# Kernel tuning notes

Hardware: AMD Instinct MI355X
Metric: run time of the kernel (lower is better)

Reference implementation:

```python
import jax, jax.numpy as jnp
import numpy as np

N = 100000  # nodes
E = 1600000  # edges
F_IN = 512
H = 128
C = 40
L = 8
ALPHA = 0.1
THETA = 0.5


def setup_inputs() -> dict:
    key = jax.random.key(0)
    ks = jax.random.split(key, 8)
    x = jax.random.normal(ks[0], (N, F_IN), dtype=jnp.float32)
    edge_index = jax.random.randint(ks[1], (2, E), 0, N, dtype=jnp.int32)
    edge_weight = jax.random.uniform(ks[2], (E,), dtype=jnp.float32)
    W0 = jax.random.normal(ks[3], (F_IN, H), dtype=jnp.float32) * 0.05
    b0 = jnp.zeros((H,), dtype=jnp.float32)
    convW = jax.random.normal(ks[4], (L, H, H), dtype=jnp.float32) * 0.05
    W1 = jax.random.normal(ks[5], (H, C), dtype=jnp.float32) * 0.05
    b1 = jnp.zeros((C,), dtype=jnp.float32)
    return {"x": x, "edge_index": edge_index, "edge_weight": edge_weight,
            "W0": W0, "b0": b0, "convW": convW, "W1": W1, "b1": b1}


def reference(x, edge_index, edge_weight, W0, b0, convW, W1, b1):
    # eval mode, dropout=0.0 -> dropout is identity
    src, dst = edge_index[0], edge_index[1]
    h = jnp.maximum(x @ W0 + b0, 0.0)  # [N, H]
    x0 = h  # initial residual
    # GCN2Conv beta per layer: log(theta/layer + 1), layer = 1..L
    betas = jnp.log(THETA / jnp.arange(1, L + 1, dtype=jnp.float32) + 1.0)

    def layer(h, inputs):
        W, beta = inputs  # W: [H, H]
        # sparse adjacency propagation: sum_j A_ij * h_j
        msgs = h[src] * edge_weight[:, None]  # [E, H]
        agg = jax.ops.segment_sum(msgs, dst, num_segments=N)  # [N, H]
        # initial residual mixing + identity mapping (shared_weights=True)
        out = (1.0 - ALPHA) * agg + ALPHA * x0
        out = (1.0 - beta) * out + beta * (out @ W)
        return jnp.maximum(out, 0.0), None

    h, _ = jax.lax.scan(layer, h, (convW, betas))
    logits = h @ W1 + b1  # [N, C]
    return jax.nn.log_softmax(logits, axis=-1)
```

## Files before the change

kernel.cpp:

```cpp
#include <hip/hip_runtime.h>
#include <hip/hip_bf16.h>
#include <cmath>

#define NN 100000
#define NE 1600000
#define FIN 512
#define HD 128
#define NC 40
#define NL 8
#define NBK 196
#define P1B 256
#define CHUNK ((NE + P1B - 1) / P1B)

typedef __attribute__((ext_vector_type(8))) short bh8;
typedef __attribute__((ext_vector_type(4))) float f4;
typedef __attribute__((ext_vector_type(4))) unsigned int u4;
typedef __attribute__((ext_vector_type(2))) unsigned int u2;

__device__ __forceinline__ float bflo(unsigned p){ return __uint_as_float(p << 16); }
__device__ __forceinline__ float bfhi(unsigned p){ return __uint_as_float(p & 0xffff0000u); }
__device__ __forceinline__ unsigned short f2bf(float f){
  unsigned u = __float_as_uint(f);
  u += 0x7fffu + ((u >> 16) & 1u);
  return (unsigned short)(u >> 16);
}
__device__ __forceinline__ unsigned pack2(float a, float b){
  return (unsigned)f2bf(a) | ((unsigned)f2bf(b) << 16);
}

__global__ __launch_bounds__(256) void k_hist(const int* __restrict__ dst,
                                              int* __restrict__ bcnt){
  __shared__ int h[256];
  int t = threadIdx.x;
  h[t] = 0;
  __syncthreads();
  int lo = blockIdx.x * CHUNK;
  int hi = lo + CHUNK < NE ? lo + CHUNK : NE;
  for (int i = lo + t; i < hi; i += 256)
    atomicAdd(&h[dst[i] >> 9], 1);
  __syncthreads();
  if (h[t]) atomicAdd(&bcnt[t], h[t]);
}

__global__ void k_bscan(const int* __restrict__ bcnt, int* __restrict__ gbase,
                        int* __restrict__ gcur, int* __restrict__ offs){
  int t = threadIdx.x;
  int carry = 0;
  for (int base = 0; base < 256; base += 64){
    int v = bcnt[base + t];
    int orig = v;
    #pragma unroll
    for (int off = 1; off < 64; off <<= 1){
      int u = __shfl_up(v, off);
      if (t >= off) v += u;
    }
    int excl = carry + v - orig;
    gbase[base + t] = excl;
    gcur[base + t] = excl;
    carry += __shfl(v, 63);
  }
  if (t == 0){ gbase[256] = carry; offs[NN] = NE; }
}

__global__ __launch_bounds__(256) void k_part(const int* __restrict__ src,
                                              const int* __restrict__ dst,
                                              const float* __restrict__ w,
                                              int* __restrict__ gcur,
                                              u2* __restrict__ tmp){
  __shared__ int h[256];
  __shared__ int base[256];
  int t = threadIdx.x;
  h[t] = 0;
  __syncthreads();
  int lo = blockIdx.x * CHUNK;
  int hi = lo + CHUNK < NE ? lo + CHUNK : NE;
  for (int i = lo + t; i < hi; i += 256)
    atomicAdd(&h[dst[i] >> 9], 1);
  __syncthreads();
  int cnt = h[t];
  if (cnt) base[t] = atomicAdd(&gcur[t], cnt);
  h[t] = 0;
  __syncthreads();
  for (int i = lo + t; i < hi; i += 256){
    int d = dst[i];
    int bk = d >> 9;
    int r = atomicAdd(&h[bk], 1);
    u2 v = { (unsigned)src[i] | ((unsigned)(d & 511) << 17), __float_as_uint(w[i]) };
    tmp[base[bk] + r] = v;
  }
}

__global__ __launch_bounds__(256) void k_place(const u2* __restrict__ tmp,
                                               const int* __restrict__ gbase,
                                               int* __restrict__ offs,
                                               u2* __restrict__ epk){
  __shared__ int h[512];
  __shared__ int lofs[512];
  int b = blockIdx.x;
  int t = threadIdx.x;
  int e0 = gbase[b], e1 = gbase[b + 1];
  h[t] = 0; h[t + 256] = 0;
  __syncthreads();
  for (int i = e0 + t; i < e1; i += 256)
    atomicAdd(&h[tmp[i].x >> 17], 1);
  __syncthreads();
  if (t < 64){
    int carry = 0;
    for (int base = 0; base < 512; base += 64){
      int v = h[base + t];
      int orig = v;
      #pragma unroll
      for (int off = 1; off < 64; off <<= 1){
        int u = __shfl_up(v, off);
        if (t >= off) v += u;
      }
      lofs[base + t] = carry + v - orig;
      carry += __shfl(v, 63);
    }
  }
  __syncthreads();
  int d = b * 512 + t;
  if (d < NN) offs[d] = e0 + lofs[t];
  int d2 = b * 512 + 256 + t;
  if (d2 < NN) offs[d2] = e0 + lofs[256 + t];
  h[t] = 0; h[t + 256] = 0;
  __syncthreads();
  for (int i = e0 + t; i < e1; i += 256){
    u2 v = tmp[i];
    int d9 = v.x >> 17;
    int r = atomicAdd(&h[d9], 1);
    u2 o = { v.x & 0x1FFFFu, v.y };
    epk[e0 + lofs[d9] + r] = o;
  }
}

__global__ void k_twt_all(const float* __restrict__ W0, const float* __restrict__ cW,
                          const float* __restrict__ W1, unsigned short* __restrict__ out){
  const int n0 = FIN * HD;
  const int n1 = NL * HD * HD;
  const int total = n0 + n1 + 48 * HD;
  for (int i = blockIdx.x * blockDim.x + threadIdx.x; i < total; i += gridDim.x * blockDim.x){
    float v;
    if (i < n0){
      int c = i / FIN, k = i % FIN;
      v = W0[(size_t)k * HD + c];
    } else if (i < n0 + n1){
      int j = i - n0;
      int l = j / (HD * HD), r = j % (HD * HD);
      int c = r / HD, k = r % HD;
      v = cW[(size_t)l * HD * HD + k * HD + c];
    } else {
      int j = i - n0 - n1;
      int c = j / HD, k = j % HD;
      v = (c < NC) ? W1[(size_t)k * NC + c] : 0.f;
    }
    out[i] = f2bf(v);
  }
}

__global__ __launch_bounds__(256) void k_gemm0(const float* __restrict__ X,
                                               const unsigned short* __restrict__ Wt,
                                               const float* __restrict__ b0,
                                               unsigned* __restrict__ Ha,
                                               unsigned* __restrict__ Hb, int n){
  __shared__ __attribute__((aligned(16))) char lds[33792];
  char* ldsA = lds;
  char* ldsW = lds + 8192;
  float* ldsO = (float*)lds;
  int t = threadIdx.x;
  int w = t >> 6, lane = t & 63;
  int rowBase = blockIdx.x * 64;
  f4 acc[8];
  #pragma unroll
  for (int i = 0; i < 8; i++) acc[i] = (f4)0.f;

  for (int kk = 0; kk < 8; kk++){
    #pragma unroll
    for (int iter = 0; iter < 2; iter++){
      int r = t / 8 + iter * 32;
      int kc = (t % 8) * 8;
      int grow = rowBase + r;
      float4 f0 = {0,0,0,0}, f1 = {0,0,0,0};
      if (grow < n){
        const float4* p = (const float4*)(X + (size_t)grow * FIN + kk * 64 + kc);
        f0 = p[0]; f1 = p[1];
      }
      u4 pv = { pack2(f0.x, f0.y), pack2(f0.z, f0.w), pack2(f1.x, f1.y), pack2(f1.z, f1.w) };
      *(u4*)(ldsA + r * 128 + ((kc * 2) ^ ((r & 7) << 4))) = pv;
    }
    #pragma unroll
    for (int iter = 0; iter < 4; iter++){
      int c = t / 8 + iter * 32;
      int kc = (t % 8) * 8;
      bh8 v = *(const bh8*)(Wt + (size_t)c * FIN + kk * 64 + kc);
      *(bh8*)(ldsW + c * 128 + ((kc * 2) ^ ((c & 7) << 4))) = v;
    }
    __syncthreads();
    int rowf = (w << 4) + (lane & 15);
    #pragma unroll
    for (int ks = 0; ks < 2; ks++){
      bh8 fa = *(const bh8*)(ldsA + rowf * 128 + ((ks * 64 + (lane >> 4) * 16) ^ ((rowf & 7) << 4)));
      #pragma unroll
      for (int ct = 0; ct < 8; ct++){
        int colf = (ct << 4) + (lane & 15);
        bh8 fb = *(const bh8*)(ldsW + colf * 128 + ((ks * 64 + (lane >> 4) * 16) ^ ((colf & 7) << 4)));
        acc[ct] = __builtin_amdgcn_mfma_f32_16x16x32_bf16(fa, fb, acc[ct], 0, 0, 0);
      }
    }
    __syncthreads();
  }
  #pragma unroll
  for (int ct = 0; ct < 8; ct++){
    int colf = (ct << 4) + (lane & 15);
    float bb = b0[colf];
    #pragma unroll
    for (int i = 0; i < 4; i++){
      int r = (w << 4) + ((lane >> 4) << 2) + i;
      float v = acc[ct][i] + bb;
      ldsO[r * 132 + colf] = v > 0.f ? v : 0.f;
    }
  }
  __syncthreads();
  #pragma unroll
  for (int iter = 0; iter < 4; iter++){
    int r = iter * 16 + t / 16;
    int c8 = (t % 16) * 8;
    int grow = rowBase + r;
    if (grow < n){
      float* p = &ldsO[r * 132 + c8];
      u4 pv = { pack2(p[0], p[1]), pack2(p[2], p[3]), pack2(p[4], p[5]), pack2(p[6], p[7]) };
      *(u4*)(Ha + (size_t)grow * 64 + (t % 16) * 4) = pv;
      *(u4*)(Hb + (size_t)grow * 64 + (t % 16) * 4) = pv;
    }
  }
}

__global__ __launch_bounds__(512) void k_layer(const unsigned* __restrict__ Hin,
                                               const unsigned* __restrict__ X0,
                                               const int* __restrict__ offs,
                                               const u2* __restrict__ epk,
                                               const unsigned short* __restrict__ Wt,
                                               float beta,
                                               unsigned* __restrict__ Hout, int n){
  __shared__ __attribute__((aligned(16))) char ldsA[16384];
  int t = threadIdx.x;
  int w = t >> 6, lane = t & 63;
  int q = lane >> 4, l16 = lane & 15;
  int quadId = (w << 2) + q;
  int rowBase = blockIdx.x * 64;

  #pragma unroll
  for (int rr = 0; rr < 2; rr++){
    int lr = (quadId << 1) + rr;
    int d = rowBase + lr;
    bool act = d < n;
    int e0 = act ? offs[d] : 0;
    int e1 = act ? offs[d + 1] : 0;
    float a0=0.f,a1=0.f,a2=0.f,a3=0.f,a4=0.f,a5=0.f,a6=0.f,a7=0.f;
    int e = e0;
    for (; e + 7 < e1; e += 8){
      #pragma unroll
      for (int j = 0; j < 8; j++){
        u2 pe = epk[e + j];
        float wf = __uint_as_float(pe.y);
        u4 r = *(const u4*)(Hin + (size_t)pe.x * 64 + l16 * 4);
        a0 += wf * bflo(r.x); a1 += wf * bfhi(r.x);
        a2 += wf * bflo(r.y); a3 += wf * bfhi(r.y);
        a4 += wf * bflo(r.z); a5 += wf * bfhi(r.z);
        a6 += wf * bflo(r.w); a7 += wf * bfhi(r.w);
      }
    }
    for (; e < e1; e++){
      u2 pe = epk[e];
      float wf = __uint_as_float(pe.y);
      u4 r = *(const u4*)(Hin + (size_t)pe.x * 64 + l16 * 4);
      a0 += wf * bflo(r.x); a1 += wf * bfhi(r.x);
      a2 += wf * bflo(r.y); a3 += wf * bfhi(r.y);
      a4 += wf * bflo(r.z); a5 += wf * bfhi(r.z);
      a6 += wf * bflo(r.w); a7 += wf * bfhi(r.w);
    }
    u4 ov = { 0u, 0u, 0u, 0u };
    if (act){
      u4 xp = *(const u4*)(X0 + (size_t)d * 64 + l16 * 4);
      float v0 = 0.9f*a0 + 0.1f*bflo(xp.x), v1 = 0.9f*a1 + 0.1f*bfhi(xp.x);
      float v2 = 0.9f*a2 + 0.1f*bflo(xp.y), v3 = 0.9f*a3 + 0.1f*bfhi(xp.y);
      float v4 = 0.9f*a4 + 0.1f*bflo(xp.z), v5 = 0.9f*a5 + 0.1f*bfhi(xp.z);
      float v6 = 0.9f*a6 + 0.1f*bflo(xp.w), v7 = 0.9f*a7 + 0.1f*bfhi(xp.w);
      ov = (u4){ pack2(v0,v1), pack2(v2,v3), pack2(v4,v5), pack2(v6,v7) };
    }
    *(u4*)(ldsA + lr * 256 + ((l16 * 16) ^ ((lr & 7) << 4))) = ov;
  }
  __syncthreads();

  f4 acc[4];
  #pragma unroll
  for (int i = 0; i < 4; i++) acc[i] = (f4)0.f;
  int rowf = ((w & 3) << 4) + l16;
  int colBase = (w >> 2) << 6;
  #pragma unroll
  for (int ks = 0; ks < 4; ks++){
    bh8 fa = *(const bh8*)(ldsA + rowf * 256 + ((ks * 64 + q * 16) ^ ((rowf & 7) << 4)));
    #pragma unroll
    for (int ct = 0; ct < 4; ct++){
      int colf = colBase + (ct << 4) + l16;
      bh8 fb = *(const bh8*)(Wt + (size_t)colf * HD + ks * 32 + q * 8);
      acc[ct] = __builtin_amdgcn_mfma_f32_16x16x32_bf16(fa, fb, acc[ct], 0, 0, 0);
    }
  }

  #pragma unroll
  for (int ct = 0; ct < 4; ct++){
    int colf = colBase + (ct << 4) + l16;
    #pragma unroll
    for (int i = 0; i < 4; i++){
      int r = ((w & 3) << 4) + (q << 2) + i;
      char* addr = ldsA + r * 256 + ((colf * 2) ^ ((r & 7) << 4));
      unsigned short tv = *(const unsigned short*)addr;
      float tf = __uint_as_float(((unsigned)tv) << 16);
      float v = (1.f - beta) * tf + beta * acc[ct][i];
      *(unsigned short*)addr = f2bf(v > 0.f ? v : 0.f);
    }
  }
  __syncthreads();

  #pragma unroll
  for (int iter = 0; iter < 2; iter++){
    int r = iter * 32 + t / 16;
    int kc = (t % 16) * 8;
    int grow = rowBase + r;
    if (grow < n){
      bh8 v = *(const bh8*)(ldsA + r * 256 + ((kc * 2) ^ ((r & 7) << 4)));
      *(bh8*)((unsigned short*)Hout + (size_t)grow * HD + kc) = v;
    }
  }
}

__global__ __launch_bounds__(256) void k_final(const unsigned* __restrict__ H,
                                               const unsigned short* __restrict__ W1t,
                                               const float* __restrict__ b1,
                                               float* __restrict__ out, int n){
  __shared__ __attribute__((aligned(16))) char lds[16384 + 12288];
  char* ldsA = lds;
  char* ldsW = lds + 16384;
  int t = threadIdx.x;
  int w = t >> 6, lane = t & 63;
  int l15 = lane & 15;
  int rowBase = blockIdx.x * 64;
  const unsigned short* Hs = (const unsigned short*)H;

  #pragma unroll
  for (int iter = 0; iter < 4; iter++){
    int r = t / 16 + iter * 16;
    int kc = (t % 16) * 8;
    int grow = rowBase + r;
    bh8 v = (bh8)(short)0;
    if (grow < n) v = *(const bh8*)(Hs + (size_t)grow * HD + kc);
    *(bh8*)(ldsA + r * 256 + ((kc * 2) ^ ((r & 7) << 4))) = v;
  }
  #pragma unroll
  for (int iter = 0; iter < 3; iter++){
    int c = t / 16 + iter * 16;
    int kc = (t % 16) * 8;
    bh8 v = *(const bh8*)(W1t + (size_t)c * HD + kc);
    *(bh8*)(ldsW + c * 256 + ((kc * 2) ^ ((c & 7) << 4))) = v;
  }
  __syncthreads();

  f4 acc[3];
  #pragma unroll
  for (int i = 0; i < 3; i++) acc[i] = (f4)0.f;
  int rowf = (w << 4) + l15;
  #pragma unroll
  for (int ks = 0; ks < 4; ks++){
    bh8 fa = *(const bh8*)(ldsA + rowf * 256 + ((ks * 64 + (lane >> 4) * 16) ^ ((rowf & 7) << 4)));
    #pragma unroll
    for (int ct = 0; ct < 3; ct++){
      int colf = (ct << 4) + l15;
      bh8 fb = *(const bh8*)(ldsW + colf * 256 + ((ks * 64 + (lane >> 4) * 16) ^ ((colf & 7) << 4)));
      acc[ct] = __builtin_amdgcn_mfma_f32_16x16x32_bf16(fa, fb, acc[ct], 0, 0, 0);
    }
  }

  float bias0 = b1[l15];
  float bias1 = b1[16 + l15];
  bool v2ok = (l15 < 8);
  float bias2 = v2ok ? b1[32 + l15] : 0.f;

  #pragma unroll
  for (int i = 0; i < 4; i++){
    int r = rowBase + (w << 4) + ((lane >> 4) << 2) + i;
    float v0 = acc[0][i] + bias0;
    float v1 = acc[1][i] + bias1;
    float v2 = v2ok ? (acc[2][i] + bias2) : -1e30f;
    float m = fmaxf(fmaxf(v0, v1), v2);
    #pragma unroll
    for (int off = 1; off < 16; off <<= 1) m = fmaxf(m, __shfl_xor(m, off));
    float e0 = __expf(v0 - m), e1 = __expf(v1 - m);
    float e2 = v2ok ? __expf(v2 - m) : 0.f;
    float s = e0 + e1 + e2;
    #pragma unroll
    for (int off = 1; off < 16; off <<= 1) s += __shfl_xor(s, off);
    float ls = m + __logf(s);
    if (r < n){
      out[(size_t)r * NC + l15] = v0 - ls;
      out[(size_t)r * NC + 16 + l15] = v1 - ls;
      if (v2ok) out[(size_t)r * NC + 32 + l15] = v2 - ls;
    }
  }
}

extern "C" void kernel_launch(void* const* d_in, const int* in_sizes, int n_in,
                              void* d_out, int out_size, void* d_ws, size_t ws_size,
                              hipStream_t stream){
  const float* x  = (const float*)d_in[0];
  const int*   ei = (const int*)d_in[1];
  const float* ew = (const float*)d_in[2];
  const float* W0 = (const float*)d_in[3];
  const float* b0 = (const float*)d_in[4];
  const float* cW = (const float*)d_in[5];
  const float* W1 = (const float*)d_in[6];
  const float* b1 = (const float*)d_in[7];
  float* out = (float*)d_out;
  const int* src = ei;
  const int* dst = ei + NE;

  char* ws = (char*)d_ws;
  size_t off = 0;
  auto alloc = [&](size_t bytes) -> char* {
    char* p = ws + off;
    off += (bytes + 255) & ~(size_t)255;
    return p;
  };
  unsigned* x0b = (unsigned*)alloc((size_t)NN * 64 * 4);
  unsigned* hbA = (unsigned*)alloc((size_t)NN * 64 * 4);
  unsigned* hbB = (unsigned*)alloc((size_t)NN * 64 * 4);
  unsigned short* wbuf = (unsigned short*)alloc(((size_t)FIN * HD + (size_t)NL * HD * HD + 48 * HD) * 2);
  unsigned short* W0t = wbuf;
  unsigned short* cWt = wbuf + (size_t)FIN * HD;
  unsigned short* W1t = cWt + (size_t)NL * HD * HD;
  int*   offs  = (int*)alloc((size_t)(NN + 1) * 4);
  int*   bcnt  = (int*)alloc(256 * 4);
  int*   gbase = (int*)alloc(257 * 4);
  int*   gcur  = (int*)alloc(256 * 4);
  u2*    tmp   = (u2*)alloc((size_t)NE * 8);
  u2*    epk   = (u2*)alloc((size_t)NE * 8);

  (void)hipMemsetAsync(bcnt, 0, 256 * 4, stream);
  hipLaunchKernelGGL(k_hist, dim3(P1B), dim3(256), 0, stream, dst, bcnt);
  hipLaunchKernelGGL(k_bscan, dim3(1), dim3(64), 0, stream, bcnt, gbase, gcur, offs);
  hipLaunchKernelGGL(k_part, dim3(P1B), dim3(256), 0, stream, src, dst, ew, gcur, tmp);
  hipLaunchKernelGGL(k_place, dim3(NBK), dim3(256), 0, stream, tmp, gbase, offs, epk);
  hipLaunchKernelGGL(k_twt_all, dim3(256), dim3(256), 0, stream, W0, cW, W1, wbuf);

  int gblocks = (NN + 63) / 64;
  hipLaunchKernelGGL(k_gemm0, dim3(gblocks), dim3(256), 0, stream, x, W0t, b0, x0b, hbA, NN);
  for (int l = 0; l < NL; l++){
    float beta = logf(0.5f / (float)(l + 1) + 1.0f);
    const unsigned* hin = (l & 1) ? hbB : hbA;
    unsigned* hout = (l & 1) ? hbA : hbB;
    hipLaunchKernelGGL(k_layer, dim3(gblocks), dim3(512), 0, stream,
                       hin, x0b, offs, epk, cWt + (size_t)l * HD * HD, beta, hout, NN);
  }
  hipLaunchKernelGGL(k_final, dim3(gblocks), dim3(256), 0, stream, hbA, W1t, b1, out, NN);
}
```

Baseline: 1.000 ms.

## Slice hidden features into 8 column planes and split aggregation from layer GEMM

Hidden and residual buffers are stored as 8 column slices of 16 features each (32 bytes per node), so each aggregation block gathers one slice. The slice-major order of blocks is meant to keep one slice's 3.2 MB working set resident in cache during the random gather. The fused per-layer kernel becomes a gather-only kernel that writes an intermediate buffer and a separate MFMA GEMM kernel that reads it back. This adds a kernel launch and an extra write and read of the intermediate per layer. Gathers also become 4-byte loads per lane instead of 16-byte vectors.

```diff
diff --git a/kernel.cpp b/kernel.cpp
--- a/kernel.cpp
+++ b/kernel.cpp
@@ -11,6 +11,8 @@
 #define NBK 196
 #define P1B 256
 #define CHUNK ((NE + P1B - 1) / P1B)
+#define ATILE 512
+#define NTILE ((NN + ATILE - 1) / ATILE)
 
 typedef __attribute__((ext_vector_type(8))) short bh8;
 typedef __attribute__((ext_vector_type(4))) float f4;
@@ -221,99 +223,105 @@
     }
   }
   __syncthreads();
-  #pragma unroll
-  for (int iter = 0; iter < 4; iter++){
-    int r = iter * 16 + t / 16;
-    int c8 = (t % 16) * 8;
-    int grow = rowBase + r;
+  int r2 = t >> 2, p = t & 3;
+  #pragma unroll
+  for (int s = 0; s < 8; s++){
+    int grow = rowBase + r2;
     if (grow < n){
-      float* p = &ldsO[r * 132 + c8];
-      u4 pv = { pack2(p[0], p[1]), pack2(p[2], p[3]), pack2(p[4], p[5]), pack2(p[6], p[7]) };
-      *(u4*)(Ha + (size_t)grow * 64 + (t % 16) * 4) = pv;
-      *(u4*)(Hb + (size_t)grow * 64 + (t % 16) * 4) = pv;
-    }
-  }
-}
-
-__global__ __launch_bounds__(512) void k_layer(const unsigned* __restrict__ Hin,
-                                               const unsigned* __restrict__ X0,
-                                               const int* __restrict__ offs,
-                                               const u2* __restrict__ epk,
+      float* pp = &ldsO[r2 * 132 + s * 16 + p * 4];
+      u2 pv = { pack2(pp[0], pp[1]), pack2(pp[2], pp[3]) };
+      *(u2*)(Ha + (size_t)s * NN * 8 + (size_t)grow * 8 + p * 2) = pv;
+      *(u2*)(Hb + (size_t)s * NN * 8 + (size_t)grow * 8 + p * 2) = pv;
+    }
+  }
+}
+
+__global__ __launch_bounds__(256) void k_agg(const unsigned* __restrict__ Hs,
+                                             const unsigned* __restrict__ X0s,
+                                             const int* __restrict__ offs,
+                                             const u2* __restrict__ epk,
+                                             unsigned* __restrict__ Ts, int n){
+  int b = blockIdx.x;
+  int s = b & 7;
+  int tile = b >> 3;
+  int t = threadIdx.x;
+  int g = t >> 3;
+  int j = t & 7;
+  const unsigned* Hb = Hs + (size_t)s * NN * 8;
+  const unsigned* Xb = X0s + (size_t)s * NN * 8;
+  unsigned* Tb = Ts + (size_t)s * NN * 8;
+  int d0 = tile * ATILE + g * 16;
+  #pragma unroll 1
+  for (int dd = 0; dd < 16; dd++){
+    int d = d0 + dd;
+    if (d >= n) break;
+    int e0 = offs[d], e1 = offs[d + 1];
+    float ax = 0.f, ay = 0.f;
+    int e = e0;
+    for (; e + 3 < e1; e += 4){
+      u2 p0 = epk[e], p1 = epk[e + 1], p2 = epk[e + 2], p3 = epk[e + 3];
+      unsigned h0 = Hb[(size_t)p0.x * 8 + j];
+      unsigned h1 = Hb[(size_t)p1.x * 8 + j];
+      unsigned h2 = Hb[(size_t)p2.x * 8 + j];
+      unsigned h3 = Hb[(size_t)p3.x * 8 + j];
+      float w0 = __uint_as_float(p0.y), w1 = __uint_as_float(p1.y);
+      float w2 = __uint_as_float(p2.y), w3 = __uint_as_float(p3.y);
+      ax += w0*bflo(h0) + w1*bflo(h1) + w2*bflo(h2) + w3*bflo(h3);
+      ay += w0*bfhi(h0) + w1*bfhi(h1) + w2*bfhi(h2) + w3*bfhi(h3);
+    }
+    for (; e < e1; e++){
+      u2 pe = epk[e];
+      unsigned h = Hb[(size_t)pe.x * 8 + j];
+      float wf = __uint_as_float(pe.y);
+      ax += wf * bflo(h); ay += wf * bfhi(h);
+    }
+    unsigned xv = Xb[(size_t)d * 8 + j];
+    float vx = 0.9f * ax + 0.1f * bflo(xv);
+    float vy = 0.9f * ay + 0.1f * bfhi(xv);
+    Tb[(size_t)d * 8 + j] = pack2(vx, vy);
+  }
+}
+
+__global__ __launch_bounds__(256) void k_gemmL(const unsigned* __restrict__ Ts,
                                                const unsigned short* __restrict__ Wt,
                                                float beta,
-                                               unsigned* __restrict__ Hout, int n){
+                                               unsigned* __restrict__ Hs, int n){
   __shared__ __attribute__((aligned(16))) char ldsA[16384];
   int t = threadIdx.x;
   int w = t >> 6, lane = t & 63;
   int q = lane >> 4, l16 = lane & 15;
-  int quadId = (w << 2) + q;
   int rowBase = blockIdx.x * 64;
-
-  #pragma unroll
-  for (int rr = 0; rr < 2; rr++){
-    int lr = (quadId << 1) + rr;
-    int d = rowBase + lr;
-    bool act = d < n;
-    int e0 = act ? offs[d] : 0;
-    int e1 = act ? offs[d + 1] : 0;
-    float a0=0.f,a1=0.f,a2=0.f,a3=0.f,a4=0.f,a5=0.f,a6=0.f,a7=0.f;
-    int e = e0;
-    for (; e + 7 < e1; e += 8){
-      #pragma unroll
-      for (int j = 0; j < 8; j++){
-        u2 pe = epk[e + j];
-        float wf = __uint_as_float(pe.y);
-        u4 r = *(const u4*)(Hin + (size_t)pe.x * 64 + l16 * 4);
-        a0 += wf * bflo(r.x); a1 += wf * bfhi(r.x);
-        a2 += wf * bflo(r.y); a3 += wf * bfhi(r.y);
-        a4 += wf * bflo(r.z); a5 += wf * bfhi(r.z);
-        a6 += wf * bflo(r.w); a7 += wf * bfhi(r.w);
-      }
-    }
-    for (; e < e1; e++){
-      u2 pe = epk[e];
-      float wf = __uint_as_float(pe.y);
-      u4 r = *(const u4*)(Hin + (size_t)pe.x * 64 + l16 * 4);
-      a0 += wf * bflo(r.x); a1 += wf * bfhi(r.x);
-      a2 += wf * bflo(r.y); a3 += wf * bfhi(r.y);
-      a4 += wf * bflo(r.z); a5 += wf * bfhi(r.z);
-      a6 += wf * bflo(r.w); a7 += wf * bfhi(r.w);
-    }
-    u4 ov = { 0u, 0u, 0u, 0u };
-    if (act){
-      u4 xp = *(const u4*)(X0 + (size_t)d * 64 + l16 * 4);
-      float v0 = 0.9f*a0 + 0.1f*bflo(xp.x), v1 = 0.9f*a1 + 0.1f*bfhi(xp.x);
-      float v2 = 0.9f*a2 + 0.1f*bflo(xp.y), v3 = 0.9f*a3 + 0.1f*bfhi(xp.y);
-      float v4 = 0.9f*a4 + 0.1f*bflo(xp.z), v5 = 0.9f*a5 + 0.1f*bfhi(xp.z);
-      float v6 = 0.9f*a6 + 0.1f*bflo(xp.w), v7 = 0.9f*a7 + 0.1f*bfhi(xp.w);
-      ov = (u4){ pack2(v0,v1), pack2(v2,v3), pack2(v4,v5), pack2(v6,v7) };
-    }
-    *(u4*)(ldsA + lr * 256 + ((l16 * 16) ^ ((lr & 7) << 4))) = ov;
-  }
-  __syncthreads();
-
-  f4 acc[4];
-  #pragma unroll
-  for (int i = 0; i < 4; i++) acc[i] = (f4)0.f;
-  int rowf = ((w & 3) << 4) + l16;
-  int colBase = (w >> 2) << 6;
+  int r2 = t >> 2, p = t & 3;
+
+  #pragma unroll
+  for (int s = 0; s < 8; s++){
+    int grow = rowBase + r2;
+    u2 v = { 0u, 0u };
+    if (grow < n) v = *(const u2*)(Ts + (size_t)s * NN * 8 + (size_t)grow * 8 + p * 2);
+    *(u2*)(ldsA + r2 * 256 + ((s * 32 + p * 8) ^ ((r2 & 7) << 4))) = v;
+  }
+
+  f4 acc[8];
+  #pragma unroll
+  for (int i = 0; i < 8; i++) acc[i] = (f4)0.f;
+  int rowf = (w << 4) + l16;
   #pragma unroll
   for (int ks = 0; ks < 4; ks++){
     bh8 fa = *(const bh8*)(ldsA + rowf * 256 + ((ks * 64 + q * 16) ^ ((rowf & 7) << 4)));
     #pragma unroll
-    for (int ct = 0; ct < 4; ct++){
-      int colf = colBase + (ct << 4) + l16;
+    for (int ct = 0; ct < 8; ct++){
+      int colf = (ct << 4) + l16;
       bh8 fb = *(const bh8*)(Wt + (size_t)colf * HD + ks * 32 + q * 8);
       acc[ct] = __builtin_amdgcn_mfma_f32_16x16x32_bf16(fa, fb, acc[ct], 0, 0, 0);
     }
   }
 
   #pragma unroll
-  for (int ct = 0; ct < 4; ct++){
-    int colf = colBase + (ct << 4) + l16;
+  for (int ct = 0; ct < 8; ct++){
+    int colf = (ct << 4) + l16;
     #pragma unroll
     for (int i = 0; i < 4; i++){
-      int r = ((w & 3) << 4) + (q << 2) + i;
+      int r = (w << 4) + (q << 2) + i;
       char* addr = ldsA + r * 256 + ((colf * 2) ^ ((r & 7) << 4));
       unsigned short tv = *(const unsigned short*)addr;
       float tf = __uint_as_float(((unsigned)tv) << 16);
@@ -324,18 +332,16 @@
   __syncthreads();
 
   #pragma unroll
-  for (int iter = 0; iter < 2; iter++){
-    int r = iter * 32 + t / 16;
-    int kc = (t % 16) * 8;
-    int grow = rowBase + r;
+  for (int s = 0; s < 8; s++){
+    int grow = rowBase + r2;
     if (grow < n){
-      bh8 v = *(const bh8*)(ldsA + r * 256 + ((kc * 2) ^ ((r & 7) << 4)));
-      *(bh8*)((unsigned short*)Hout + (size_t)grow * HD + kc) = v;
-    }
-  }
-}
-
-__global__ __launch_bounds__(256) void k_final(const unsigned* __restrict__ H,
+      u2 v = *(const u2*)(ldsA + r2 * 256 + ((s * 32 + p * 8) ^ ((r2 & 7) << 4)));
+      *(u2*)(Hs + (size_t)s * NN * 8 + (size_t)grow * 8 + p * 2) = v;
+    }
+  }
+}
+
+__global__ __launch_bounds__(256) void k_final(const unsigned* __restrict__ Hs,
                                                const unsigned short* __restrict__ W1t,
                                                const float* __restrict__ b1,
                                                float* __restrict__ out, int n){
@@ -346,16 +352,14 @@
   int w = t >> 6, lane = t & 63;
   int l15 = lane & 15;
   int rowBase = blockIdx.x * 64;
-  const unsigned short* Hs = (const unsigned short*)H;
-
-  #pragma unroll
-  for (int iter = 0; iter < 4; iter++){
-    int r = t / 16 + iter * 16;
-    int kc = (t % 16) * 8;
-    int grow = rowBase + r;
-    bh8 v = (bh8)(short)0;
-    if (grow < n) v = *(const bh8*)(Hs + (size_t)grow * HD + kc);
-    *(bh8*)(ldsA + r * 256 + ((kc * 2) ^ ((r & 7) << 4))) = v;
+  int r2 = t >> 2, p = t & 3;
+
+  #pragma unroll
+  for (int s = 0; s < 8; s++){
+    int grow = rowBase + r2;
+    u2 v = { 0u, 0u };
+    if (grow < n) v = *(const u2*)(Hs + (size_t)s * NN * 8 + (size_t)grow * 8 + p * 2);
+    *(u2*)(ldsA + r2 * 256 + ((s * 32 + p * 8) ^ ((r2 & 7) << 4))) = v;
   }
   #pragma unroll
   for (int iter = 0; iter < 3; iter++){
@@ -434,6 +438,7 @@
   unsigned* x0b = (unsigned*)alloc((size_t)NN * 64 * 4);
   unsigned* hbA = (unsigned*)alloc((size_t)NN * 64 * 4);
   unsigned* hbB = (unsigned*)alloc((size_t)NN * 64 * 4);
+  unsigned* tb  = (unsigned*)alloc((size_t)NN * 64 * 4);
   unsigned short* wbuf = (unsigned short*)alloc(((size_t)FIN * HD + (size_t)NL * HD * HD + 48 * HD) * 2);
   unsigned short* W0t = wbuf;
   unsigned short* cWt = wbuf + (size_t)FIN * HD;
@@ -458,8 +463,10 @@
     float beta = logf(0.5f / (float)(l + 1) + 1.0f);
     const unsigned* hin = (l & 1) ? hbB : hbA;
     unsigned* hout = (l & 1) ? hbA : hbB;
-    hipLaunchKernelGGL(k_layer, dim3(gblocks), dim3(512), 0, stream,
-                       hin, x0b, offs, epk, cWt + (size_t)l * HD * HD, beta, hout, NN);
+    hipLaunchKernelGGL(k_agg, dim3(NTILE * 8), dim3(256), 0, stream,
+                       hin, x0b, offs, epk, tb, NN);
+    hipLaunchKernelGGL(k_gemmL, dim3(gblocks), dim3(256), 0, stream,
+                       tb, cWt + (size_t)l * HD * HD, beta, hout, NN);
   }
   hipLaunchKernelGGL(k_final, dim3(gblocks), dim3(256), 0, stream, hbA, W1t, b1, out, NN);
 }
```

Result: slower. 1.550 ms (+55.0%).

## Split fused layer kernel into grid-stride aggregation and separate MFMA GEMM

Applied to the files above, without the earlier changes.

The fused per-layer kernel (gather-aggregate into LDS, then MFMA transform) is split into two kernels. k_agg is a persistent grid-stride kernel with one 16-lane group per node, using no LDS and no barriers. It writes the residual-mixed bf16 result to a new global buffer. k_gemmL reads that buffer into LDS and runs the 128x128 transform with each wave covering all output columns. This aims to free the memory-bound gather from the GEMM's LDS, barrier and occupancy limits and to balance irregular degrees better. The cost is an extra global write and read of an N×128 bf16 tensor plus a second launch per layer.

```diff
diff --git a/kernel.cpp b/kernel.cpp
--- a/kernel.cpp
+++ b/kernel.cpp
@@ -235,27 +235,17 @@
   }
 }
 
-__global__ __launch_bounds__(512) void k_layer(const unsigned* __restrict__ Hin,
-                                               const unsigned* __restrict__ X0,
-                                               const int* __restrict__ offs,
-                                               const u2* __restrict__ epk,
-                                               const unsigned short* __restrict__ Wt,
-                                               float beta,
-                                               unsigned* __restrict__ Hout, int n){
-  __shared__ __attribute__((aligned(16))) char ldsA[16384];
-  int t = threadIdx.x;
-  int w = t >> 6, lane = t & 63;
-  int q = lane >> 4, l16 = lane & 15;
-  int quadId = (w << 2) + q;
-  int rowBase = blockIdx.x * 64;
-
-  #pragma unroll
-  for (int rr = 0; rr < 2; rr++){
-    int lr = (quadId << 1) + rr;
-    int d = rowBase + lr;
-    bool act = d < n;
-    int e0 = act ? offs[d] : 0;
-    int e1 = act ? offs[d + 1] : 0;
+__global__ __launch_bounds__(256) void k_agg(const unsigned* __restrict__ H,
+                                             const unsigned* __restrict__ X0,
+                                             const int* __restrict__ offs,
+                                             const u2* __restrict__ epk,
+                                             unsigned* __restrict__ T, int n){
+  int t = threadIdx.x;
+  int qid = (blockIdx.x << 4) + (t >> 4);
+  int l16 = t & 15;
+  int nq = gridDim.x << 4;
+  for (int d = qid; d < n; d += nq){
+    int e0 = offs[d], e1 = offs[d + 1];
     float a0=0.f,a1=0.f,a2=0.f,a3=0.f,a4=0.f,a5=0.f,a6=0.f,a7=0.f;
     int e = e0;
     for (; e + 7 < e1; e += 8){
@@ -263,7 +253,7 @@
       for (int j = 0; j < 8; j++){
         u2 pe = epk[e + j];
         float wf = __uint_as_float(pe.y);
-        u4 r = *(const u4*)(Hin + (size_t)pe.x * 64 + l16 * 4);
+        u4 r = *(const u4*)(H + (size_t)pe.x * 64 + l16 * 4);
         a0 += wf * bflo(r.x); a1 += wf * bfhi(r.x);
         a2 += wf * bflo(r.y); a3 += wf * bfhi(r.y);
         a4 += wf * bflo(r.z); a5 += wf * bfhi(r.z);
@@ -273,47 +263,63 @@
     for (; e < e1; e++){
       u2 pe = epk[e];
       float wf = __uint_as_float(pe.y);
-      u4 r = *(const u4*)(Hin + (size_t)pe.x * 64 + l16 * 4);
+      u4 r = *(const u4*)(H + (size_t)pe.x * 64 + l16 * 4);
       a0 += wf * bflo(r.x); a1 += wf * bfhi(r.x);
       a2 += wf * bflo(r.y); a3 += wf * bfhi(r.y);
       a4 += wf * bflo(r.z); a5 += wf * bfhi(r.z);
       a6 += wf * bflo(r.w); a7 += wf * bfhi(r.w);
     }
-    u4 ov = { 0u, 0u, 0u, 0u };
-    if (act){
-      u4 xp = *(const u4*)(X0 + (size_t)d * 64 + l16 * 4);
-      float v0 = 0.9f*a0 + 0.1f*bflo(xp.x), v1 = 0.9f*a1 + 0.1f*bfhi(xp.x);
-      float v2 = 0.9f*a2 + 0.1f*bflo(xp.y), v3 = 0.9f*a3 + 0.1f*bfhi(xp.y);
-      float v4 = 0.9f*a4 + 0.1f*bflo(xp.z), v5 = 0.9f*a5 + 0.1f*bfhi(xp.z);
-      float v6 = 0.9f*a6 + 0.1f*bflo(xp.w), v7 = 0.9f*a7 + 0.1f*bfhi(xp.w);
-      ov = (u4){ pack2(v0,v1), pack2(v2,v3), pack2(v4,v5), pack2(v6,v7) };
-    }
-    *(u4*)(ldsA + lr * 256 + ((l16 * 16) ^ ((lr & 7) << 4))) = ov;
-  }
-  __syncthreads();
-
-  f4 acc[4];
-  #pragma unroll
-  for (int i = 0; i < 4; i++) acc[i] = (f4)0.f;
-  int rowf = ((w & 3) << 4) + l16;
-  int colBase = (w >> 2) << 6;
+    u4 xp = *(const u4*)(X0 + (size_t)d * 64 + l16 * 4);
+    float v0 = 0.9f*a0 + 0.1f*bflo(xp.x), v1 = 0.9f*a1 + 0.1f*bfhi(xp.x);
+    float v2 = 0.9f*a2 + 0.1f*bflo(xp.y), v3 = 0.9f*a3 + 0.1f*bfhi(xp.y);
+    float v4 = 0.9f*a4 + 0.1f*bflo(xp.z), v5 = 0.9f*a5 + 0.1f*bfhi(xp.z);
+    float v6 = 0.9f*a6 + 0.1f*bflo(xp.w), v7 = 0.9f*a7 + 0.1f*bfhi(xp.w);
+    u4 ov = { pack2(v0,v1), pack2(v2,v3), pack2(v4,v5), pack2(v6,v7) };
+    *(u4*)(T + (size_t)d * 64 + l16 * 4) = ov;
+  }
+}
+
+__global__ __launch_bounds__(256) void k_gemmL(const unsigned short* __restrict__ A,
+                                               const unsigned short* __restrict__ Wt,
+                                               float beta,
+                                               unsigned* __restrict__ Hout, int n){
+  __shared__ __attribute__((aligned(16))) char ldsA[16384];
+  int t = threadIdx.x;
+  int w = t >> 6, lane = t & 63;
+  int q = lane >> 4, l16 = lane & 15;
+  int rowBase = blockIdx.x * 64;
+
+  #pragma unroll
+  for (int it = 0; it < 4; it++){
+    int lr = (w << 4) + (lane >> 2);
+    int j = it * 4 + (lane & 3);
+    int grow = rowBase + lr;
+    bh8 v = (bh8)(short)0;
+    if (grow < n) v = *(const bh8*)(A + (size_t)grow * HD + j * 8);
+    *(bh8*)(ldsA + lr * 256 + ((j * 16) ^ ((lr & 7) << 4))) = v;
+  }
+
+  f4 acc[8];
+  #pragma unroll
+  for (int i = 0; i < 8; i++) acc[i] = (f4)0.f;
+  int rowf = (w << 4) + l16;
   #pragma unroll
   for (int ks = 0; ks < 4; ks++){
     bh8 fa = *(const bh8*)(ldsA + rowf * 256 + ((ks * 64 + q * 16) ^ ((rowf & 7) << 4)));
     #pragma unroll
-    for (int ct = 0; ct < 4; ct++){
-      int colf = colBase + (ct << 4) + l16;
+    for (int ct = 0; ct < 8; ct++){
+      int colf = (ct << 4) + l16;
       bh8 fb = *(const bh8*)(Wt + (size_t)colf * HD + ks * 32 + q * 8);
       acc[ct] = __builtin_amdgcn_mfma_f32_16x16x32_bf16(fa, fb, acc[ct], 0, 0, 0);
     }
   }
 
   #pragma unroll
-  for (int ct = 0; ct < 4; ct++){
-    int colf = colBase + (ct << 4) + l16;
+  for (int ct = 0; ct < 8; ct++){
+    int colf = (ct << 4) + l16;
     #pragma unroll
     for (int i = 0; i < 4; i++){
-      int r = ((w & 3) << 4) + (q << 2) + i;
+      int r = (w << 4) + (q << 2) + i;
       char* addr = ldsA + r * 256 + ((colf * 2) ^ ((r & 7) << 4));
       unsigned short tv = *(const unsigned short*)addr;
       float tf = __uint_as_float(((unsigned)tv) << 16);
@@ -324,8 +330,8 @@
   __syncthreads();
 
   #pragma unroll
-  for (int iter = 0; iter < 2; iter++){
-    int r = iter * 32 + t / 16;
+  for (int iter = 0; iter < 4; iter++){
+    int r = iter * 16 + t / 16;
     int kc = (t % 16) * 8;
     int grow = rowBase + r;
     if (grow < n){
@@ -434,6 +440,7 @@
   unsigned* x0b = (unsigned*)alloc((size_t)NN * 64 * 4);
   unsigned* hbA = (unsigned*)alloc((size_t)NN * 64 * 4);
   unsigned* hbB = (unsigned*)alloc((size_t)NN * 64 * 4);
+  unsigned* tb  = (unsigned*)alloc((size_t)NN * 64 * 4);
   unsigned short* wbuf = (unsigned short*)alloc(((size_t)FIN * HD + (size_t)NL * HD * HD + 48 * HD) * 2);
   unsigned short* W0t = wbuf;
   unsigned short* cWt = wbuf + (size_t)FIN * HD;
@@ -458,8 +465,10 @@
     float beta = logf(0.5f / (float)(l + 1) + 1.0f);
     const unsigned* hin = (l & 1) ? hbB : hbA;
     unsigned* hout = (l & 1) ? hbA : hbB;
-    hipLaunchKernelGGL(k_layer, dim3(gblocks), dim3(512), 0, stream,
-                       hin, x0b, offs, epk, cWt + (size_t)l * HD * HD, beta, hout, NN);
+    hipLaunchKernelGGL(k_agg, dim3(2048), dim3(256), 0, stream,
+                       hin, x0b, offs, epk, tb, NN);
+    hipLaunchKernelGGL(k_gemmL, dim3(gblocks), dim3(256), 0, stream,
+                       (const unsigned short*)tb, cWt + (size_t)l * HD * HD, beta, hout, NN);
   }
   hipLaunchKernelGGL(k_final, dim3(gblocks), dim3(256), 0, stream, hbA, W1t, b1, out, NN);
 }
```

Result: slower. 1.031 ms (+3.1%).

## Fuse final classifier and log-softmax into last layer kernel; pad edge loop

Applied to the files above, without the earlier changes.

The separate final kernel is removed. On the last propagation layer, k_layer now applies W1, adds the bias and computes log-softmax straight from the LDS tile, so the final H is never written to global memory and read back, and one launch goes away. The edge gather loop also drops its scalar remainder loop. It now runs padded groups of 8 with masked loads, where masked entries use index 0 and weight 0, so out-of-range lanes re-read node 0 instead of skipping the work. W1 fragments are read directly from global memory with no LDS staging, and only 4 of the 8 waves do the classifier work.

```diff
diff --git a/kernel.cpp b/kernel.cpp
--- a/kernel.cpp
+++ b/kernel.cpp
@@ -241,7 +241,10 @@
                                                const u2* __restrict__ epk,
                                                const unsigned short* __restrict__ Wt,
                                                float beta,
-                                               unsigned* __restrict__ Hout, int n){
+                                               unsigned* __restrict__ Hout, int n,
+                                               const unsigned short* __restrict__ W1t,
+                                               const float* __restrict__ b1,
+                                               float* __restrict__ out, int last){
   __shared__ __attribute__((aligned(16))) char ldsA[16384];
   int t = threadIdx.x;
   int w = t >> 6, lane = t & 63;
@@ -257,11 +260,12 @@
     int e0 = act ? offs[d] : 0;
     int e1 = act ? offs[d + 1] : 0;
     float a0=0.f,a1=0.f,a2=0.f,a3=0.f,a4=0.f,a5=0.f,a6=0.f,a7=0.f;
-    int e = e0;
-    for (; e + 7 < e1; e += 8){
+    for (int e = e0; e < e1; e += 8){
       #pragma unroll
       for (int j = 0; j < 8; j++){
-        u2 pe = epk[e + j];
+        int ee = e + j;
+        u2 pe = { 0u, 0u };
+        if (ee < e1) pe = epk[ee];
         float wf = __uint_as_float(pe.y);
         u4 r = *(const u4*)(Hin + (size_t)pe.x * 64 + l16 * 4);
         a0 += wf * bflo(r.x); a1 += wf * bfhi(r.x);
@@ -269,15 +273,6 @@
         a4 += wf * bflo(r.z); a5 += wf * bfhi(r.z);
         a6 += wf * bflo(r.w); a7 += wf * bfhi(r.w);
       }
-    }
-    for (; e < e1; e++){
-      u2 pe = epk[e];
-      float wf = __uint_as_float(pe.y);
-      u4 r = *(const u4*)(Hin + (size_t)pe.x * 64 + l16 * 4);
-      a0 += wf * bflo(r.x); a1 += wf * bfhi(r.x);
-      a2 += wf * bflo(r.y); a3 += wf * bfhi(r.y);
-      a4 += wf * bflo(r.z); a5 += wf * bfhi(r.z);
-      a6 += wf * bflo(r.w); a7 += wf * bfhi(r.w);
     }
     u4 ov = { 0u, 0u, 0u, 0u };
     if (act){
@@ -323,88 +318,57 @@
   }
   __syncthreads();
 
-  #pragma unroll
-  for (int iter = 0; iter < 2; iter++){
-    int r = iter * 32 + t / 16;
-    int kc = (t % 16) * 8;
-    int grow = rowBase + r;
-    if (grow < n){
-      bh8 v = *(const bh8*)(ldsA + r * 256 + ((kc * 2) ^ ((r & 7) << 4)));
-      *(bh8*)((unsigned short*)Hout + (size_t)grow * HD + kc) = v;
-    }
-  }
-}
-
-__global__ __launch_bounds__(256) void k_final(const unsigned* __restrict__ H,
-                                               const unsigned short* __restrict__ W1t,
-                                               const float* __restrict__ b1,
-                                               float* __restrict__ out, int n){
-  __shared__ __attribute__((aligned(16))) char lds[16384 + 12288];
-  char* ldsA = lds;
-  char* ldsW = lds + 16384;
-  int t = threadIdx.x;
-  int w = t >> 6, lane = t & 63;
-  int l15 = lane & 15;
-  int rowBase = blockIdx.x * 64;
-  const unsigned short* Hs = (const unsigned short*)H;
-
-  #pragma unroll
-  for (int iter = 0; iter < 4; iter++){
-    int r = t / 16 + iter * 16;
-    int kc = (t % 16) * 8;
-    int grow = rowBase + r;
-    bh8 v = (bh8)(short)0;
-    if (grow < n) v = *(const bh8*)(Hs + (size_t)grow * HD + kc);
-    *(bh8*)(ldsA + r * 256 + ((kc * 2) ^ ((r & 7) << 4))) = v;
-  }
-  #pragma unroll
-  for (int iter = 0; iter < 3; iter++){
-    int c = t / 16 + iter * 16;
-    int kc = (t % 16) * 8;
-    bh8 v = *(const bh8*)(W1t + (size_t)c * HD + kc);
-    *(bh8*)(ldsW + c * 256 + ((kc * 2) ^ ((c & 7) << 4))) = v;
-  }
-  __syncthreads();
-
-  f4 acc[3];
-  #pragma unroll
-  for (int i = 0; i < 3; i++) acc[i] = (f4)0.f;
-  int rowf = (w << 4) + l15;
-  #pragma unroll
-  for (int ks = 0; ks < 4; ks++){
-    bh8 fa = *(const bh8*)(ldsA + rowf * 256 + ((ks * 64 + (lane >> 4) * 16) ^ ((rowf & 7) << 4)));
-    #pragma unroll
-    for (int ct = 0; ct < 3; ct++){
-      int colf = (ct << 4) + l15;
-      bh8 fb = *(const bh8*)(ldsW + colf * 256 + ((ks * 64 + (lane >> 4) * 16) ^ ((colf & 7) << 4)));
-      acc[ct] = __builtin_amdgcn_mfma_f32_16x16x32_bf16(fa, fb, acc[ct], 0, 0, 0);
-    }
-  }
-
-  float bias0 = b1[l15];
-  float bias1 = b1[16 + l15];
-  bool v2ok = (l15 < 8);
-  float bias2 = v2ok ? b1[32 + l15] : 0.f;
-
-  #pragma unroll
-  for (int i = 0; i < 4; i++){
-    int r = rowBase + (w << 4) + ((lane >> 4) << 2) + i;
-    float v0 = acc[0][i] + bias0;
-    float v1 = acc[1][i] + bias1;
-    float v2 = v2ok ? (acc[2][i] + bias2) : -1e30f;
-    float m = fmaxf(fmaxf(v0, v1), v2);
-    #pragma unroll
-    for (int off = 1; off < 16; off <<= 1) m = fmaxf(m, __shfl_xor(m, off));
-    float e0 = __expf(v0 - m), e1 = __expf(v1 - m);
-    float e2 = v2ok ? __expf(v2 - m) : 0.f;
-    float s = e0 + e1 + e2;
-    #pragma unroll
-    for (int off = 1; off < 16; off <<= 1) s += __shfl_xor(s, off);
-    float ls = m + __logf(s);
-    if (r < n){
-      out[(size_t)r * NC + l15] = v0 - ls;
-      out[(size_t)r * NC + 16 + l15] = v1 - ls;
-      if (v2ok) out[(size_t)r * NC + 32 + l15] = v2 - ls;
+  if (!last){
+    #pragma unroll
+    for (int iter = 0; iter < 2; iter++){
+      int r = iter * 32 + t / 16;
+      int kc = (t % 16) * 8;
+      int grow = rowBase + r;
+      if (grow < n){
+        bh8 v = *(const bh8*)(ldsA + r * 256 + ((kc * 2) ^ ((r & 7) << 4)));
+        *(bh8*)((unsigned short*)Hout + (size_t)grow * HD + kc) = v;
+      }
+    }
+  } else if (w < 4){
+    int l15 = lane & 15;
+    f4 hacc[3];
+    #pragma unroll
+    for (int i = 0; i < 3; i++) hacc[i] = (f4)0.f;
+    int hrow = (w << 4) + l15;
+    #pragma unroll
+    for (int ks = 0; ks < 4; ks++){
+      bh8 fa = *(const bh8*)(ldsA + hrow * 256 + ((ks * 64 + (lane >> 4) * 16) ^ ((hrow & 7) << 4)));
+      #pragma unroll
+      for (int ct = 0; ct < 3; ct++){
+        int colf = (ct << 4) + l15;
+        bh8 fb = *(const bh8*)(W1t + (size_t)colf * HD + ks * 32 + (lane >> 4) * 8);
+        hacc[ct] = __builtin_amdgcn_mfma_f32_16x16x32_bf16(fa, fb, hacc[ct], 0, 0, 0);
+      }
+    }
+    float bias0 = b1[l15];
+    float bias1 = b1[16 + l15];
+    bool v2ok = (l15 < 8);
+    float bias2 = v2ok ? b1[32 + l15] : 0.f;
+    #pragma unroll
+    for (int i = 0; i < 4; i++){
+      int r = rowBase + (w << 4) + ((lane >> 4) << 2) + i;
+      float v0 = hacc[0][i] + bias0;
+      float v1 = hacc[1][i] + bias1;
+      float v2 = v2ok ? (hacc[2][i] + bias2) : -1e30f;
+      float m = fmaxf(fmaxf(v0, v1), v2);
+      #pragma unroll
+      for (int off = 1; off < 16; off <<= 1) m = fmaxf(m, __shfl_xor(m, off));
+      float e0 = __expf(v0 - m), e1 = __expf(v1 - m);
+      float e2 = v2ok ? __expf(v2 - m) : 0.f;
+      float s = e0 + e1 + e2;
+      #pragma unroll
+      for (int off = 1; off < 16; off <<= 1) s += __shfl_xor(s, off);
+      float ls = m + __logf(s);
+      if (r < n){
+        out[(size_t)r * NC + l15] = v0 - ls;
+        out[(size_t)r * NC + 16 + l15] = v1 - ls;
+        if (v2ok) out[(size_t)r * NC + 32 + l15] = v2 - ls;
+      }
     }
   }
 }
@@ -459,7 +423,7 @@
     const unsigned* hin = (l & 1) ? hbB : hbA;
     unsigned* hout = (l & 1) ? hbA : hbB;
     hipLaunchKernelGGL(k_layer, dim3(gblocks), dim3(512), 0, stream,
-                       hin, x0b, offs, epk, cWt + (size_t)l * HD * HD, beta, hout, NN);
-  }
-  hipLaunchKernelGGL(k_final, dim3(gblocks), dim3(256), 0, stream, hbA, W1t, b1, out, NN);
-}
+                       hin, x0b, offs, epk, cWt + (size_t)l * HD * HD, beta, hout, NN,
+                       W1t, b1, out, (l == NL - 1) ? 1 : 0);
+  }
+}
```

Result: no change. 992.0 us, median of 2 (-0.8%).
